# Performance work log

Measured on AMD Instinct MI355X. Metric: run time of the kernel, lower is better.

## Reference

```python
import jax, jax.numpy as jnp
import numpy as np

NEG = -1e30  # stand-in for -inf on the H-attention diagonal (matches INF helper)


def _conv1x1(w, b, x):
    # w: [O, C], x: [B, C, H, W]
    return jnp.einsum('oc,bchw->bohw', w, x) + b[None, :, None, None]


def _cc_attn(q, k, v):
    """Criss-cross attention: q,k [B,Cq,H,W], v [B,C,H,W] -> [B,C,H,W]."""
    B, _, H, W = q.shape
    # column (H) energies: query at (h,w) attends to keys at (h', w)
    eH = jnp.einsum('bchw,bcjw->bhwj', q, k)  # [B,H,W,H]
    eye = jnp.eye(H, dtype=bool)[None, :, None, :]
    eH = jnp.where(eye, NEG, eH)  # mask h==h' (self counted once via W pass)
    # row (W) energies: query at (h,w) attends to keys at (h, w')
    eW = jnp.einsum('bchw,bchj->bhwj', q, k)  # [B,H,W,W]
    att = jax.nn.softmax(jnp.concatenate([eH, eW], axis=3), axis=3)  # [B,H,W,H+W]
    aH, aW = att[..., :H], att[..., H:]
    outH = jnp.einsum('bhwj,bcjw->bchw', aH, v)
    outW = jnp.einsum('bhwj,bchj->bchw', aW, v)
    return outH + outW


def setup_inputs() -> dict:
    key = jax.random.key(0)
    ks = jax.random.split(key, 14)
    B, C, H, W = 8, 256, 96, 96
    Cq = C // 8
    n = jax.random.normal
    return {
        'x': n(ks[0], (B, C, H, W), jnp.float32),
        'y': n(ks[1], (B, C, H, W), jnp.float32),
        'Wq': n(ks[2], (Cq, C), jnp.float32) * 0.05,
        'bq': n(ks[3], (Cq,), jnp.float32) * 0.05,
        'Wk': n(ks[4], (Cq, C), jnp.float32) * 0.05,
        'bk': n(ks[5], (Cq,), jnp.float32) * 0.05,
        'Wv': n(ks[6], (C, C), jnp.float32) * 0.05,
        'bv': n(ks[7], (C,), jnp.float32) * 0.05,
        'gamma1': n(ks[8], (1,), jnp.float32) * 0.1,
        'gamma2': n(ks[9], (1,), jnp.float32) * 0.1,
        'Wd': n(ks[10], (2 * C, 1, 3, 3), jnp.float32) * 0.1,  # depthwise, groups=2C
        'bd': n(ks[11], (2 * C,), jnp.float32) * 0.05,
        'Wp': n(ks[12], (C, 2 * C), jnp.float32) * 0.05,  # pointwise 1x1
        'bp': n(ks[13], (C,), jnp.float32) * 0.05,
    }


def reference(x, y, Wq, bq, Wk, bk, Wv, bv, gamma1, gamma2, Wd, bd, Wp, bp):
    qx = _conv1x1(Wq, bq, x)
    kx = _conv1x1(Wk, bk, x)
    vx = _conv1x1(Wv, bv, x)
    qy = _conv1x1(Wq, bq, y)
    ky = _conv1x1(Wk, bk, y)
    vy = _conv1x1(Wv, bv, y)
    # pass 1: attention weights from x, values from y
    out1 = gamma1[0] * _cc_attn(qx, kx, vy) + x
    # pass 2: attention weights from y, values from x
    out2 = gamma2[0] * _cc_attn(qy, ky, vx) + y
    z = jnp.concatenate([out1, out2], axis=1)  # [B, 2C, H, W]
    # depthwise 3x3 (groups = 2C), padding 1
    z = jax.lax.conv_general_dilated(
        z, Wd, window_strides=(1, 1), padding='SAME',
        feature_group_count=z.shape[1],
        dimension_numbers=('NCHW', 'OIHW', 'NCHW')) + bd[None, :, None, None]
    # pointwise 1x1 then LeakyReLU (torch default negative_slope=0.01)
    z = _conv1x1(Wp, bp, z)
    return jax.nn.leaky_relu(z, negative_slope=0.01)
```

## Files before the change

kernel.cpp:

```cpp
#include <hip/hip_runtime.h>
#include <hip/hip_bf16.h>

constexpr int kB  = 8;
constexpr int kC  = 256;
constexpr int kCq = 32;
constexpr int kH  = 96;
constexpr int kW  = 96;
constexpr int kP  = kH * kW;

using bf16x8 = __attribute__((ext_vector_type(8))) short;
using bf16x4 = __attribute__((ext_vector_type(4))) short;
using f32x4  = __attribute__((ext_vector_type(4))) float;

__device__ inline bf16x8 ld_lds8(const __hip_bfloat16* p) {
    bf16x4 lo = *(const bf16x4*)p;
    bf16x4 hi = *(const bf16x4*)(p + 4);
    return __builtin_shufflevector(lo, hi, 0, 1, 2, 3, 4, 5, 6, 7);
}

__global__ __launch_bounds__(256) void w_convert(
    const float* __restrict__ Wq, const float* __restrict__ Wk,
    const float* __restrict__ Wv,
    __hip_bfloat16* __restrict__ Wqkb, __hip_bfloat16* __restrict__ Wvb)
{
    const int i = blockIdx.x * 256 + threadIdx.x;
    if (i < 8192)       Wqkb[i] = __float2bfloat16(Wq[i]);
    else if (i < 16384) Wqkb[i] = __float2bfloat16(Wk[i - 8192]);
    else                Wvb[i - 16384] = __float2bfloat16(Wv[i - 16384]);
}

__global__ __launch_bounds__(256) void qkv_mfma(
    const float* __restrict__ in_qk, const float* __restrict__ in_v,
    const __hip_bfloat16* __restrict__ Wqkb, const __hip_bfloat16* __restrict__ Wvb,
    const float* __restrict__ bq, const float* __restrict__ bk,
    const float* __restrict__ bv,
    __hip_bfloat16* __restrict__ Qbh, __hip_bfloat16* __restrict__ Qbl,
    __hip_bfloat16* __restrict__ Kbh, __hip_bfloat16* __restrict__ Kbl,
    __hip_bfloat16* __restrict__ Vpm, __hip_bfloat16* __restrict__ Vhw)
{
    const int b = blockIdx.y;
    const int t = threadIdx.x;
    const int wv = t >> 6, l = t & 63;
    const int n = l & 15, q = l >> 4;
    const int p = blockIdx.x * 64 + wv * 16 + n;
    const size_t bP = (size_t)b * kP;

    const float* __restrict__ xq = in_qk + (size_t)b * kC * kP + p;
    const float* __restrict__ xv = in_v  + (size_t)b * kC * kP + p;

    f32x4 acc[20];
#pragma unroll
    for (int i = 0; i < 20; i++) acc[i] = (f32x4)0.f;

    for (int kc = 0; kc < 8; kc++) {
        const int c0 = kc * 32 + q * 8;
        float fq[8], fv[8];
#pragma unroll
        for (int j = 0; j < 8; j++) fq[j] = xq[(size_t)(c0 + j) * kP];
#pragma unroll
        for (int j = 0; j < 8; j++) fv[j] = xv[(size_t)(c0 + j) * kP];
        union { bf16x8 v; __hip_bfloat16 h[8]; } bfq, bfv;
#pragma unroll
        for (int j = 0; j < 8; j++) bfq.h[j] = __float2bfloat16(fq[j]);
#pragma unroll
        for (int j = 0; j < 8; j++) bfv.h[j] = __float2bfloat16(fv[j]);

#pragma unroll
        for (int mt = 0; mt < 4; mt++) {
            bf16x8 a = *(const bf16x8*)(Wqkb + ((mt * 16 + n) << 8) + c0);
            acc[mt] = __builtin_amdgcn_mfma_f32_16x16x32_bf16(a, bfq.v, acc[mt], 0, 0, 0);
        }
#pragma unroll
        for (int mt = 0; mt < 16; mt++) {
            bf16x8 a = *(const bf16x8*)(Wvb + ((mt * 16 + n) << 8) + c0);
            acc[4 + mt] = __builtin_amdgcn_mfma_f32_16x16x32_bf16(a, bfv.v, acc[4 + mt], 0, 0, 0);
        }
    }

#pragma unroll
    for (int mt = 0; mt < 2; mt++) {
        float4 bias = *(const float4*)&bq[mt * 16 + q * 4];
        float v0 = acc[mt][0] + bias.x, v1 = acc[mt][1] + bias.y;
        float v2 = acc[mt][2] + bias.z, v3 = acc[mt][3] + bias.w;
        union { ushort4 u; __hip_bfloat16 h[4]; } hi, lo;
        float vv[4] = { v0, v1, v2, v3 };
#pragma unroll
        for (int r = 0; r < 4; r++) {
            __hip_bfloat16 h = __float2bfloat16(vv[r]);
            hi.h[r] = h;
            lo.h[r] = __float2bfloat16(vv[r] - __bfloat162float(h));
        }
        *(ushort4*)&Qbh[(bP + p) * kCq + mt * 16 + q * 4] = hi.u;
        *(ushort4*)&Qbl[(bP + p) * kCq + mt * 16 + q * 4] = lo.u;
    }
#pragma unroll
    for (int mt = 2; mt < 4; mt++) {
        float4 bias = *(const float4*)&bk[(mt - 2) * 16 + q * 4];
        float vv[4] = { acc[mt][0] + bias.x, acc[mt][1] + bias.y,
                        acc[mt][2] + bias.z, acc[mt][3] + bias.w };
        union { ushort4 u; __hip_bfloat16 h[4]; } hi, lo;
#pragma unroll
        for (int r = 0; r < 4; r++) {
            __hip_bfloat16 h = __float2bfloat16(vv[r]);
            hi.h[r] = h;
            lo.h[r] = __float2bfloat16(vv[r] - __bfloat162float(h));
        }
        *(ushort4*)&Kbh[(bP + p) * kCq + (mt - 2) * 16 + q * 4] = hi.u;
        *(ushort4*)&Kbl[(bP + p) * kCq + (mt - 2) * 16 + q * 4] = lo.u;
    }
#pragma unroll
    for (int mt = 0; mt < 16; mt++) {
        float4 bias = *(const float4*)&bv[mt * 16 + q * 4];
        float vv[4] = { acc[4 + mt][0] + bias.x, acc[4 + mt][1] + bias.y,
                        acc[4 + mt][2] + bias.z, acc[4 + mt][3] + bias.w };
        union { ushort4 u; __hip_bfloat16 h[4]; } pm;
#pragma unroll
        for (int r = 0; r < 4; r++) pm.h[r] = __float2bfloat16(vv[r]);
        *(ushort4*)&Vpm[(bP + p) * kC + mt * 16 + q * 4] = pm.u;
#pragma unroll
        for (int r = 0; r < 4; r++)
            Vhw[((size_t)b * kC + mt * 16 + q * 4 + r) * kP + p] = pm.h[r];
    }
}

__global__ __launch_bounds__(256) void cc_stats(
    const __hip_bfloat16* __restrict__ Qbh, const __hip_bfloat16* __restrict__ Qbl,
    const __hip_bfloat16* __restrict__ Kbh, const __hip_bfloat16* __restrict__ Kbl,
    float* __restrict__ Sm, float* __restrict__ Si)
{
    __shared__ __align__(16) __hip_bfloat16 QH[96][36], QLo[96][36];
    __shared__ __align__(16) __hip_bfloat16 KH[96][36], KLo[96][36];
    __shared__ __align__(16) float EL[96][97];
    const int w = blockIdx.x, b = blockIdx.y;
    const int t = threadIdx.x;
    const size_t bP = (size_t)b * kP;

    for (int idx = t; idx < 768; idx += 256) {
        int row = idx >> 3, ch = (idx & 7) * 4;
        size_t g = (bP + (size_t)row * kW + w) * kCq + ch;
        *(ushort4*)&QH[row][ch]  = *(const ushort4*)&Qbh[g];
        *(ushort4*)&QLo[row][ch] = *(const ushort4*)&Qbl[g];
        *(ushort4*)&KH[row][ch]  = *(const ushort4*)&Kbh[g];
        *(ushort4*)&KLo[row][ch] = *(const ushort4*)&Kbl[g];
    }
    __syncthreads();

    const int wv = t >> 6, l = t & 63, ln = l & 15, lq = l >> 4;
#pragma unroll
    for (int s = 0; s < 9; s++) {
        int tile = wv * 9 + s, it = tile / 6, jt = tile % 6;
        bf16x8 ah = ld_lds8(&QH[it * 16 + ln][lq * 8]);
        bf16x8 al = ld_lds8(&QLo[it * 16 + ln][lq * 8]);
        bf16x8 bh = ld_lds8(&KH[jt * 16 + ln][lq * 8]);
        bf16x8 bl = ld_lds8(&KLo[jt * 16 + ln][lq * 8]);
        f32x4 d = (f32x4)0.f;
        d = __builtin_amdgcn_mfma_f32_16x16x32_bf16(al, bh, d, 0, 0, 0);
        d = __builtin_amdgcn_mfma_f32_16x16x32_bf16(ah, bl, d, 0, 0, 0);
        d = __builtin_amdgcn_mfma_f32_16x16x32_bf16(ah, bh, d, 0, 0, 0);
#pragma unroll
        for (int r = 0; r < 4; r++)
            EL[it * 16 + lq * 4 + r][jt * 16 + ln] = d[r];
    }
    __syncthreads();

    const int sub = t & 7;
    for (int pi = t >> 3; pi < 96; pi += 32) {
        float ev[12];
        float mx = -3.0e38f;
#pragma unroll
        for (int k = 0; k < 12; k++) {
            int j = sub + 8 * k;
            float e = EL[pi][j];
            if (j == pi) e = -3.0e38f;
            ev[k] = e;
            mx = fmaxf(mx, e);
        }
#pragma unroll
        for (int k = 1; k < 8; k <<= 1) mx = fmaxf(mx, __shfl_xor(mx, k, 8));
        float ss = 0.f;
#pragma unroll
        for (int k = 0; k < 12; k++) ss += __expf(ev[k] - mx);
#pragma unroll
        for (int k = 1; k < 8; k <<= 1) ss += __shfl_xor(ss, k, 8);
        if (sub == 0) {
            Sm[bP + (size_t)pi * kW + w] = mx;
            Si[bP + (size_t)pi * kW + w] = ss;
        }
    }
}

__global__ __launch_bounds__(256) void cc_pass1(
    const __hip_bfloat16* __restrict__ Qbh, const __hip_bfloat16* __restrict__ Qbl,
    const __hip_bfloat16* __restrict__ Kbh, const __hip_bfloat16* __restrict__ Kbl,
    const __hip_bfloat16* __restrict__ Vhw,
    const float* __restrict__ res_in, const float* __restrict__ gamma_p,
    __hip_bfloat16* __restrict__ Zb, float* __restrict__ Sm, float* __restrict__ Si,
    int s_off)
{
    __shared__ __align__(16) __hip_bfloat16 QH[32][36], QLo[32][36];
    __shared__ __align__(16) __hip_bfloat16 KH[96][36], KLo[96][36];
    __shared__ __align__(16) float EL[32][97];
    __shared__ __align__(16) __hip_bfloat16 attL[32][100];
    __shared__ __align__(16) float rs[32][260];
    const int wt = blockIdx.x, h = blockIdx.y, b = blockIdx.z;
    const int w0 = wt * 32;
    const int t = threadIdx.x;
    const size_t bP = (size_t)b * kP;

    {
        int row = t >> 3, ch = (t & 7) * 4;
        size_t g = (bP + (size_t)h * kW + w0 + row) * kCq + ch;
        *(ushort4*)&QH[row][ch]  = *(const ushort4*)&Qbh[g];
        *(ushort4*)&QLo[row][ch] = *(const ushort4*)&Qbl[g];
    }
    for (int idx = t; idx < 768; idx += 256) {
        int row = idx >> 3, ch = (idx & 7) * 4;
        size_t g = (bP + (size_t)h * kW + row) * kCq + ch;
        *(ushort4*)&KH[row][ch]  = *(const ushort4*)&Kbh[g];
        *(ushort4*)&KLo[row][ch] = *(const ushort4*)&Kbl[g];
    }
    const float* __restrict__ res = res_in + (size_t)b * kC * kP + (size_t)h * kW + w0;
    {
        const int f4 = t & 7;
        int c2 = t >> 3;
#pragma unroll
        for (int it2 = 0; it2 < 8; it2++, c2 += 32) {
            float4 v = *(const float4*)&res[(size_t)c2 * kP + f4 * 4];
            rs[f4 * 4 + 0][c2] = v.x;
            rs[f4 * 4 + 1][c2] = v.y;
            rs[f4 * 4 + 2][c2] = v.z;
            rs[f4 * 4 + 3][c2] = v.w;
        }
    }
    __syncthreads();

    const int wv = t >> 6, l = t & 63, ln = l & 15, lq = l >> 4;
#pragma unroll
    for (int s = 0; s < 3; s++) {
        int tile = wv * 3 + s, it = tile / 6, jt = tile % 6;
        bf16x8 ah = ld_lds8(&QH[it * 16 + ln][lq * 8]);
        bf16x8 al = ld_lds8(&QLo[it * 16 + ln][lq * 8]);
        bf16x8 bh = ld_lds8(&KH[jt * 16 + ln][lq * 8]);
        bf16x8 bl = ld_lds8(&KLo[jt * 16 + ln][lq * 8]);
        f32x4 d = (f32x4)0.f;
        d = __builtin_amdgcn_mfma_f32_16x16x32_bf16(al, bh, d, 0, 0, 0);
        d = __builtin_amdgcn_mfma_f32_16x16x32_bf16(ah, bl, d, 0, 0, 0);
        d = __builtin_amdgcn_mfma_f32_16x16x32_bf16(ah, bh, d, 0, 0, 0);
#pragma unroll
        for (int r = 0; r < 4; r++)
            EL[it * 16 + lq * 4 + r][jt * 16 + ln] = d[r];
    }
    __syncthreads();

    {
        const int pi = t >> 3, sub = t & 7;
        size_t sidx = bP + (size_t)h * kW + w0 + pi;
        float mH = Sm[sidx], sH = Si[sidx];
        float ev[12];
        float mx = mH;
#pragma unroll
        for (int k = 0; k < 12; k++) {
            float e = EL[pi][sub + 8 * k];
            ev[k] = e;
            mx = fmaxf(mx, e);
        }
#pragma unroll
        for (int k = 1; k < 8; k <<= 1) mx = fmaxf(mx, __shfl_xor(mx, k, 8));
        float ss = 0.f;
#pragma unroll
        for (int k = 0; k < 12; k++) { float e = __expf(ev[k] - mx); ev[k] = e; ss += e; }
#pragma unroll
        for (int k = 1; k < 8; k <<= 1) ss += __shfl_xor(ss, k, 8);
        float stot = ss + sH * __expf(mH - mx);
        float inv = 1.0f / stot;
        if (sub == 0) { Sm[sidx] = mx; Si[sidx] = inv; }
#pragma unroll
        for (int k = 0; k < 12; k++)
            attL[pi][sub + 8 * k] = __float2bfloat16(ev[k] * inv);
    }
    __syncthreads();

    bf16x8 aF[2][3];
#pragma unroll
    for (int it = 0; it < 2; it++)
#pragma unroll
        for (int j3 = 0; j3 < 3; j3++)
            aF[it][j3] = ld_lds8(&attL[it * 16 + ln][j3 * 32 + lq * 8]);

    f32x4 acc[2][4];
#pragma unroll
    for (int it = 0; it < 2; it++)
#pragma unroll
        for (int c4 = 0; c4 < 4; c4++) acc[it][c4] = (f32x4)0.f;

#pragma unroll
    for (int c4 = 0; c4 < 4; c4++) {
        const int c = (wv * 4 + c4) * 16 + ln;
        const __hip_bfloat16* vr = Vhw + ((size_t)b * kC + c) * kP + (size_t)h * kW;
        bf16x8 bF0 = *(const bf16x8*)&vr[lq * 8];
        bf16x8 bF1 = *(const bf16x8*)&vr[32 + lq * 8];
        bf16x8 bF2 = *(const bf16x8*)&vr[64 + lq * 8];
#pragma unroll
        for (int it = 0; it < 2; it++) {
            acc[it][c4] = __builtin_amdgcn_mfma_f32_16x16x32_bf16(aF[it][0], bF0, acc[it][c4], 0, 0, 0);
            acc[it][c4] = __builtin_amdgcn_mfma_f32_16x16x32_bf16(aF[it][1], bF1, acc[it][c4], 0, 0, 0);
            acc[it][c4] = __builtin_amdgcn_mfma_f32_16x16x32_bf16(aF[it][2], bF2, acc[it][c4], 0, 0, 0);
        }
    }

    const float gamma = gamma_p[0];
#pragma unroll
    for (int c4 = 0; c4 < 4; c4++) {
        const int c = (wv * 4 + c4) * 16 + ln;
#pragma unroll
        for (int it = 0; it < 2; it++) {
#pragma unroll
            for (int r = 0; r < 4; r++) {
                int i = it * 16 + lq * 4 + r;
                float z = gamma * acc[it][c4][r] + rs[i][c];
                Zb[(bP + (size_t)h * kW + w0 + i) * 512 + s_off + c] = __float2bfloat16(z);
            }
        }
    }
}

__global__ __launch_bounds__(256) void cc_pass2(
    const __hip_bfloat16* __restrict__ Qbh, const __hip_bfloat16* __restrict__ Qbl,
    const __hip_bfloat16* __restrict__ Kbh, const __hip_bfloat16* __restrict__ Kbl,
    const __hip_bfloat16* __restrict__ Vpm,
    const float* __restrict__ gamma_p, __hip_bfloat16* __restrict__ Zb,
    const float* __restrict__ Sm, const float* __restrict__ Si, int s_off)
{
    __shared__ __align__(16) __hip_bfloat16 QH[32][36], QLo[32][36];
    __shared__ __align__(16) __hip_bfloat16 KH[96][36], KLo[96][36];
    __shared__ __align__(16) __hip_bfloat16 VL[96][260];
    __shared__ __align__(16) __hip_bfloat16 attL[32][100];
    const int ht = blockIdx.x, w = blockIdx.y, b = blockIdx.z;
    const int h0 = ht * 32;
    const int t = threadIdx.x;
    const size_t bP = (size_t)b * kP;

    {
        int row = t >> 3, ch = (t & 7) * 4;
        size_t g = (bP + (size_t)(h0 + row) * kW + w) * kCq + ch;
        *(ushort4*)&QH[row][ch]  = *(const ushort4*)&Qbh[g];
        *(ushort4*)&QLo[row][ch] = *(const ushort4*)&Qbl[g];
    }
    for (int idx = t; idx < 768; idx += 256) {
        int row = idx >> 3, ch = (idx & 7) * 4;
        size_t g = (bP + (size_t)row * kW + w) * kCq + ch;
        *(ushort4*)&KH[row][ch]  = *(const ushort4*)&Kbh[g];
        *(ushort4*)&KLo[row][ch] = *(const ushort4*)&Kbl[g];
    }
    for (int idx = t; idx < 96 * 32; idx += 256) {
        int j = idx >> 5, cg = (idx & 31) * 8;
        const ushort4* src = (const ushort4*)&Vpm[(bP + (size_t)j * kW + w) * kC + cg];
        ushort4 v0 = src[0], v1 = src[1];
        *(ushort4*)&VL[j][cg]     = v0;
        *(ushort4*)&VL[j][cg + 4] = v1;
    }
    __syncthreads();

    const int wv = t >> 6, l = t & 63, ln = l & 15, lq = l >> 4;
#pragma unroll
    for (int s = 0; s < 3; s++) {
        int tile = wv * 3 + s, it = tile / 6, jt = tile % 6;
        bf16x8 ah = ld_lds8(&QH[it * 16 + ln][lq * 8]);
        bf16x8 al = ld_lds8(&QLo[it * 16 + ln][lq * 8]);
        bf16x8 bh = ld_lds8(&KH[jt * 16 + ln][lq * 8]);
        bf16x8 bl = ld_lds8(&KLo[jt * 16 + ln][lq * 8]);
        f32x4 d = (f32x4)0.f;
        d = __builtin_amdgcn_mfma_f32_16x16x32_bf16(al, bh, d, 0, 0, 0);
        d = __builtin_amdgcn_mfma_f32_16x16x32_bf16(ah, bl, d, 0, 0, 0);
        d = __builtin_amdgcn_mfma_f32_16x16x32_bf16(ah, bh, d, 0, 0, 0);
        const int j = jt * 16 + ln;
#pragma unroll
        for (int r = 0; r < 4; r++) {
            int i = it * 16 + lq * 4 + r;
            size_t sidx = bP + (size_t)(h0 + i) * kW + w;
            float m = Sm[sidx], inv = Si[sidx];
            float a = (j == h0 + i) ? 0.f : __expf(d[r] - m) * inv;
            attL[i][j] = __float2bfloat16(a);
        }
    }
    __syncthreads();

    bf16x8 aF[2][3];
#pragma unroll
    for (int it = 0; it < 2; it++)
#pragma unroll
        for (int j3 = 0; j3 < 3; j3++)
            aF[it][j3] = ld_lds8(&attL[it * 16 + ln][j3 * 32 + lq * 8]);

    f32x4 acc[2][4];
#pragma unroll
    for (int it = 0; it < 2; it++)
#pragma unroll
        for (int c4 = 0; c4 < 4; c4++) acc[it][c4] = (f32x4)0.f;

#pragma unroll
    for (int c4 = 0; c4 < 4; c4++) {
        const int c = (wv * 4 + c4) * 16 + ln;
#pragma unroll
        for (int j3 = 0; j3 < 3; j3++) {
            union { bf16x8 v; __hip_bfloat16 h[8]; } bF;
#pragma unroll
            for (int jj = 0; jj < 8; jj++)
                bF.h[jj] = VL[j3 * 32 + lq * 8 + jj][c];
#pragma unroll
            for (int it = 0; it < 2; it++)
                acc[it][c4] = __builtin_amdgcn_mfma_f32_16x16x32_bf16(aF[it][j3], bF.v, acc[it][c4], 0, 0, 0);
        }
    }

    const float gamma = gamma_p[0];
#pragma unroll
    for (int c4 = 0; c4 < 4; c4++) {
        const int c = (wv * 4 + c4) * 16 + ln;
#pragma unroll
        for (int it = 0; it < 2; it++) {
#pragma unroll
            for (int r = 0; r < 4; r++) {
                int i = it * 16 + lq * 4 + r;
                size_t zi = (bP + (size_t)(h0 + i) * kW + w) * 512 + s_off + c;
                float old = __bfloat162float(Zb[zi]);
                Zb[zi] = __float2bfloat16(old + gamma * acc[it][c4][r]);
            }
        }
    }
}

__global__ __launch_bounds__(256) void wp_convert(
    const float* __restrict__ Wp, __hip_bfloat16* __restrict__ Wpb)
{
    const int i = blockIdx.x * 256 + threadIdx.x;
    Wpb[i] = __float2bfloat16(Wp[i]);
}

__global__ __launch_bounds__(256) void dwpw(
    const __hip_bfloat16* __restrict__ Zb,
    const float* __restrict__ Wdw, const float* __restrict__ bd,
    const __hip_bfloat16* __restrict__ Wpb, const float* __restrict__ bp,
    float* __restrict__ out)
{
    __shared__ __align__(16) char smem[33792];
    __hip_bfloat16 (*zs)[520] = (__hip_bfloat16 (*)[520])smem;

    const int wt = blockIdx.x, h = blockIdx.y, b = blockIdx.z;
    const int w0 = wt * 32;
    const int t = threadIdx.x;
    const size_t bP = (size_t)b * kP;

    {
        float wd0[9], wd1[9];
#pragma unroll
        for (int k = 0; k < 9; k++) {
            wd0[k] = Wdw[(size_t)(2 * t) * 9 + k];
            wd1[k] = Wdw[(size_t)(2 * t + 1) * 9 + k];
        }
        const float b0 = bd[2 * t], b1 = bd[2 * t + 1];
        const __hip_bfloat162* __restrict__ Zp =
            (const __hip_bfloat162*)Zb + bP * 256 + t;
        const bool rvm = (h > 0), rvp = (h < kH - 1);

#pragma unroll
        for (int j0 = 0; j0 < 32; j0 += 8) {
            float2 wf[10][3];
#pragma unroll
            for (int col = 0; col < 10; col++) {
                const int ww = w0 + j0 - 1 + col;
                const bool cv = (ww >= 0) && (ww < kW);
#pragma unroll
                for (int r = 0; r < 3; r++) {
                    const bool v = cv && (r == 1 || (r == 0 ? rvm : rvp));
                    __hip_bfloat162 z2;
                    z2.x = __ushort_as_bfloat16(0);
                    z2.y = __ushort_as_bfloat16(0);
                    if (v) z2 = Zp[(size_t)((h + r - 1) * kW + ww) * 256];
                    wf[col][r] = __bfloat1622float2(z2);
                }
            }
#pragma unroll
            for (int j = 0; j < 8; j++) {
                float a0 = b0, a1 = b1;
#pragma unroll
                for (int r = 0; r < 3; r++) {
#pragma unroll
                    for (int dw = 0; dw < 3; dw++) {
                        const float2 z = wf[j + dw][r];
                        const int k = r * 3 + dw;
                        a0 += wd0[k] * z.x;
                        a1 += wd1[k] * z.y;
                    }
                }
                __hip_bfloat162 pz;
                pz.x = __float2bfloat16(a0);
                pz.y = __float2bfloat16(a1);
                ((__hip_bfloat162*)&zs[j0 + j][0])[t] = pz;
            }
        }
    }
    __syncthreads();

    const int l = t & 63, wv = t >> 6;
    const int lo16 = l & 15, q = l >> 4;

    f32x4 acc[2][4];
#pragma unroll
    for (int mt = 0; mt < 2; mt++)
#pragma unroll
        for (int nt = 0; nt < 4; nt++) acc[mt][nt] = (f32x4)0.f;

    const bf16x8* __restrict__ Bb[4];
#pragma unroll
    for (int nt = 0; nt < 4; nt++)
        Bb[nt] = (const bf16x8*)(Wpb + (size_t)(wv * 64 + nt * 16 + lo16) * 512);

    for (int kc = 0; kc < 16; kc++) {
        bf16x8 a0 = *(const bf16x8*)&zs[lo16][kc * 32 + q * 8];
        bf16x8 a1 = *(const bf16x8*)&zs[16 + lo16][kc * 32 + q * 8];
#pragma unroll
        for (int nt = 0; nt < 4; nt++) {
            bf16x8 bf = Bb[nt][kc * 4 + q];
            acc[0][nt] = __builtin_amdgcn_mfma_f32_16x16x32_bf16(a0, bf, acc[0][nt], 0, 0, 0);
            acc[1][nt] = __builtin_amdgcn_mfma_f32_16x16x32_bf16(a1, bf, acc[1][nt], 0, 0, 0);
        }
    }
    __syncthreads();

    float* os = (float*)smem + (size_t)wv * 64 * 33;
#pragma unroll
    for (int nt = 0; nt < 4; nt++) {
        const int ol = nt * 16 + lo16;
        const float bias = bp[wv * 64 + ol];
#pragma unroll
        for (int mt = 0; mt < 2; mt++) {
#pragma unroll
            for (int r = 0; r < 4; r++) {
                float v = acc[mt][nt][r] + bias;
                v = v > 0.f ? v : 0.01f * v;
                os[ol * 33 + mt * 16 + q * 4 + r] = v;
            }
        }
    }
    __syncthreads();
    const int px = l & 31, oh = l >> 5;
    for (int j = 0; j < 32; j++) {
        const int ol = j * 2 + oh;
        out[((size_t)b * 256 + wv * 64 + ol) * kP + (size_t)h * kW + w0 + px] =
            os[ol * 33 + px];
    }
}

extern "C" void kernel_launch(void* const* d_in, const int* in_sizes, int n_in,
                              void* d_out, int out_size, void* d_ws, size_t ws_size,
                              hipStream_t stream)
{
    const float* x   = (const float*)d_in[0];
    const float* y   = (const float*)d_in[1];
    const float* Wq  = (const float*)d_in[2];
    const float* bq  = (const float*)d_in[3];
    const float* Wk  = (const float*)d_in[4];
    const float* bk  = (const float*)d_in[5];
    const float* Wv  = (const float*)d_in[6];
    const float* bv  = (const float*)d_in[7];
    const float* g1  = (const float*)d_in[8];
    const float* g2  = (const float*)d_in[9];
    const float* Wdw = (const float*)d_in[10];
    const float* bd  = (const float*)d_in[11];
    const float* Wp  = (const float*)d_in[12];
    const float* bp  = (const float*)d_in[13];
    float* out = (float*)d_out;

    char* wsb = (char*)d_ws;
    __hip_bfloat16* Zb  = (__hip_bfloat16*)wsb;
    __hip_bfloat16* Qbh = (__hip_bfloat16*)(wsb + 75497472);
    __hip_bfloat16* Qbl = Qbh + 2359296;
    __hip_bfloat16* Kbh = (__hip_bfloat16*)(wsb + 84934656);
    __hip_bfloat16* Kbl = Kbh + 2359296;
    float* Sm = (float*)(wsb + 94371840);
    float* Si = (float*)(wsb + 94666752);
    __hip_bfloat16* Wqkb = (__hip_bfloat16*)Sm;
    __hip_bfloat16* Wvb  = ((__hip_bfloat16*)Sm) + 16384;
    __hip_bfloat16* Wpb  = (__hip_bfloat16*)(wsb + 75497472);
    __hip_bfloat16* Vpm  = (__hip_bfloat16*)d_out;
    __hip_bfloat16* Vhw  = Vpm + 18874368;

    hipLaunchKernelGGL(w_convert, dim3(320), dim3(256), 0, stream,
                       Wq, Wk, Wv, Wqkb, Wvb);
    hipLaunchKernelGGL(qkv_mfma, dim3(kP / 64, kB), dim3(256), 0, stream,
                       x, y, Wqkb, Wvb, bq, bk, bv, Qbh, Qbl, Kbh, Kbl, Vpm, Vhw);
    hipLaunchKernelGGL(cc_stats, dim3(kW, kB), dim3(256), 0, stream,
                       Qbh, Qbl, Kbh, Kbl, Sm, Si);
    hipLaunchKernelGGL(cc_pass1, dim3(kW / 32, kH, kB), dim3(256), 0, stream,
                       Qbh, Qbl, Kbh, Kbl, Vhw, x, g1, Zb, Sm, Si, 0);
    hipLaunchKernelGGL(cc_pass2, dim3(kH / 32, kW, kB), dim3(256), 0, stream,
                       Qbh, Qbl, Kbh, Kbl, Vpm, g1, Zb, Sm, Si, 0);
    hipLaunchKernelGGL(w_convert, dim3(320), dim3(256), 0, stream,
                       Wq, Wk, Wv, Wqkb, Wvb);
    hipLaunchKernelGGL(qkv_mfma, dim3(kP / 64, kB), dim3(256), 0, stream,
                       y, x, Wqkb, Wvb, bq, bk, bv, Qbh, Qbl, Kbh, Kbl, Vpm, Vhw);
    hipLaunchKernelGGL(cc_stats, dim3(kW, kB), dim3(256), 0, stream,
                       Qbh, Qbl, Kbh, Kbl, Sm, Si);
    hipLaunchKernelGGL(cc_pass1, dim3(kW / 32, kH, kB), dim3(256), 0, stream,
                       Qbh, Qbl, Kbh, Kbl, Vhw, y, g2, Zb, Sm, Si, 256);
    hipLaunchKernelGGL(cc_pass2, dim3(kH / 32, kW, kB), dim3(256), 0, stream,
                       Qbh, Qbl, Kbh, Kbl, Vpm, g2, Zb, Sm, Si, 256);
    hipLaunchKernelGGL(wp_convert, dim3(512), dim3(256), 0, stream, Wp, Wpb);
    hipLaunchKernelGGL(dwpw, dim3(kW / 32, kH, kB), dim3(256), 0, stream,
                       Zb, Wdw, bd, Wpb, bp, out);
}
```

Baseline: 977.3 us.

## Stage QKV conv inputs through double-buffered LDS and coalesce Vhw stores

The QKV projection kernel now loads input activations as float4 vectors across pixels, converts them to bf16 and stages them transposed in a double-buffered LDS tile. The next channel chunk is prefetched while MFMAs run on the current one, replacing strided per-thread scalar global loads. The channel-major Vhw output is also transposed through LDS so each thread writes contiguous 16-byte rows instead of scattered 2-byte stores. The cost is about 34 KB of LDS per block and extra barriers, which may reduce occupancy.

```diff
diff --git a/kernel.cpp b/kernel.cpp
--- a/kernel.cpp
+++ b/kernel.cpp
@@ -38,52 +38,101 @@
     __hip_bfloat16* __restrict__ Kbh, __hip_bfloat16* __restrict__ Kbl,
     __hip_bfloat16* __restrict__ Vpm, __hip_bfloat16* __restrict__ Vhw)
 {
-    const int b = blockIdx.y;
-    const int t = threadIdx.x;
+    __shared__ __align__(16) char smem[34816];
+    __hip_bfloat16* sqb = (__hip_bfloat16*)smem;
+    __hip_bfloat16* svb = sqb + 2 * 64 * 36;
+    __hip_bfloat16* vt  = (__hip_bfloat16*)smem;
+
+    const int b = blockIdx.y, t = threadIdx.x;
     const int wv = t >> 6, l = t & 63;
     const int n = l & 15, q = l >> 4;
-    const int p = blockIdx.x * 64 + wv * 16 + n;
+    const int p0 = blockIdx.x * 64;
+    const int p  = p0 + wv * 16 + n;
     const size_t bP = (size_t)b * kP;
 
-    const float* __restrict__ xq = in_qk + (size_t)b * kC * kP + p;
-    const float* __restrict__ xv = in_v  + (size_t)b * kC * kP + p;
+    const float* __restrict__ xq = in_qk + (size_t)b * kC * kP + p0;
+    const float* __restrict__ xv = in_v  + (size_t)b * kC * kP + p0;
+
+    const int sc = t >> 4;
+    const int sp = (t & 15) * 4;
 
     f32x4 acc[20];
 #pragma unroll
     for (int i = 0; i < 20; i++) acc[i] = (f32x4)0.f;
 
+    {
+        float4 q0 = *(const float4*)&xq[(size_t)sc * kP + sp];
+        float4 q1 = *(const float4*)&xq[(size_t)(16 + sc) * kP + sp];
+        float4 v0 = *(const float4*)&xv[(size_t)sc * kP + sp];
+        float4 v1 = *(const float4*)&xv[(size_t)(16 + sc) * kP + sp];
+        float fq0[4] = { q0.x, q0.y, q0.z, q0.w };
+        float fq1[4] = { q1.x, q1.y, q1.z, q1.w };
+        float fv0[4] = { v0.x, v0.y, v0.z, v0.w };
+        float fv1[4] = { v1.x, v1.y, v1.z, v1.w };
+#pragma unroll
+        for (int j = 0; j < 4; j++) {
+            sqb[(sp + j) * 36 + sc]      = __float2bfloat16(fq0[j]);
+            sqb[(sp + j) * 36 + 16 + sc] = __float2bfloat16(fq1[j]);
+            svb[(sp + j) * 36 + sc]      = __float2bfloat16(fv0[j]);
+            svb[(sp + j) * 36 + 16 + sc] = __float2bfloat16(fv1[j]);
+        }
+    }
+    __syncthreads();
+
+    int cur = 0;
     for (int kc = 0; kc < 8; kc++) {
+        float4 nq0, nq1, nv0, nv1;
+        if (kc < 7) {
+            const size_t cb = (size_t)(kc + 1) * 32;
+            nq0 = *(const float4*)&xq[(cb + sc) * kP + sp];
+            nq1 = *(const float4*)&xq[(cb + 16 + sc) * kP + sp];
+            nv0 = *(const float4*)&xv[(cb + sc) * kP + sp];
+            nv1 = *(const float4*)&xv[(cb + 16 + sc) * kP + sp];
+        }
+
+        const __hip_bfloat16* sqp = sqb + cur * 2304 + (wv * 16 + n) * 36 + q * 8;
+        const __hip_bfloat16* svp = svb + cur * 2304 + (wv * 16 + n) * 36 + q * 8;
+        bf16x8 bfq = ld_lds8(sqp);
+        bf16x8 bfv = ld_lds8(svp);
         const int c0 = kc * 32 + q * 8;
-        float fq[8], fv[8];
-#pragma unroll
-        for (int j = 0; j < 8; j++) fq[j] = xq[(size_t)(c0 + j) * kP];
-#pragma unroll
-        for (int j = 0; j < 8; j++) fv[j] = xv[(size_t)(c0 + j) * kP];
-        union { bf16x8 v; __hip_bfloat16 h[8]; } bfq, bfv;
-#pragma unroll
-        for (int j = 0; j < 8; j++) bfq.h[j] = __float2bfloat16(fq[j]);
-#pragma unroll
-        for (int j = 0; j < 8; j++) bfv.h[j] = __float2bfloat16(fv[j]);
 
 #pragma unroll
         for (int mt = 0; mt < 4; mt++) {
             bf16x8 a = *(const bf16x8*)(Wqkb + ((mt * 16 + n) << 8) + c0);
-            acc[mt] = __builtin_amdgcn_mfma_f32_16x16x32_bf16(a, bfq.v, acc[mt], 0, 0, 0);
+            acc[mt] = __builtin_amdgcn_mfma_f32_16x16x32_bf16(a, bfq, acc[mt], 0, 0, 0);
         }
 #pragma unroll
         for (int mt = 0; mt < 16; mt++) {
             bf16x8 a = *(const bf16x8*)(Wvb + ((mt * 16 + n) << 8) + c0);
-            acc[4 + mt] = __builtin_amdgcn_mfma_f32_16x16x32_bf16(a, bfv.v, acc[4 + mt], 0, 0, 0);
-        }
+            acc[4 + mt] = __builtin_amdgcn_mfma_f32_16x16x32_bf16(a, bfv, acc[4 + mt], 0, 0, 0);
+        }
+
+        if (kc < 7) {
+            const int nb = cur ^ 1;
+            __hip_bfloat16* dq = sqb + nb * 2304;
+            __hip_bfloat16* dv = svb + nb * 2304;
+            float fq0[4] = { nq0.x, nq0.y, nq0.z, nq0.w };
+            float fq1[4] = { nq1.x, nq1.y, nq1.z, nq1.w };
+            float fv0[4] = { nv0.x, nv0.y, nv0.z, nv0.w };
+            float fv1[4] = { nv1.x, nv1.y, nv1.z, nv1.w };
+#pragma unroll
+            for (int j = 0; j < 4; j++) {
+                dq[(sp + j) * 36 + sc]      = __float2bfloat16(fq0[j]);
+                dq[(sp + j) * 36 + 16 + sc] = __float2bfloat16(fq1[j]);
+                dv[(sp + j) * 36 + sc]      = __float2bfloat16(fv0[j]);
+                dv[(sp + j) * 36 + 16 + sc] = __float2bfloat16(fv1[j]);
+            }
+        }
+        __syncthreads();
+        cur ^= 1;
     }
 
 #pragma unroll
     for (int mt = 0; mt < 2; mt++) {
         float4 bias = *(const float4*)&bq[mt * 16 + q * 4];
-        float v0 = acc[mt][0] + bias.x, v1 = acc[mt][1] + bias.y;
-        float v2 = acc[mt][2] + bias.z, v3 = acc[mt][3] + bias.w;
+        float vv[4] = { acc[mt][0] + bias.x, acc[mt][1] + bias.y,
+                        acc[mt][2] + bias.z, acc[mt][3] + bias.w };
         union { ushort4 u; __hip_bfloat16 h[4]; } hi, lo;
-        float vv[4] = { v0, v1, v2, v3 };
 #pragma unroll
         for (int r = 0; r < 4; r++) {
             __hip_bfloat16 h = __float2bfloat16(vv[r]);
@@ -108,6 +157,7 @@
         *(ushort4*)&Kbh[(bP + p) * kCq + (mt - 2) * 16 + q * 4] = hi.u;
         *(ushort4*)&Kbl[(bP + p) * kCq + (mt - 2) * 16 + q * 4] = lo.u;
     }
+
 #pragma unroll
     for (int mt = 0; mt < 16; mt++) {
         float4 bias = *(const float4*)&bv[mt * 16 + q * 4];
@@ -119,7 +169,17 @@
         *(ushort4*)&Vpm[(bP + p) * kC + mt * 16 + q * 4] = pm.u;
 #pragma unroll
         for (int r = 0; r < 4; r++)
-            Vhw[((size_t)b * kC + mt * 16 + q * 4 + r) * kP + p] = pm.h[r];
+            vt[(mt * 16 + q * 4 + r) * 68 + wv * 16 + n] = pm.h[r];
+    }
+    __syncthreads();
+
+    {
+        __hip_bfloat16* dst = Vhw + ((size_t)b * kC + t) * kP + p0;
+#pragma unroll
+        for (int j = 0; j < 8; j++) {
+            bf16x8 row = ld_lds8(&vt[t * 68 + j * 8]);
+            *(bf16x8*)&dst[j * 8] = row;
+        }
     }
 }
 
```

New measurement: 919.4 us. 1.06x faster.
